# Optimization experiments

Measured on AMD Instinct MI355X. Metric: run time of the kernel, lower is better.

The kernel has to match this reference:

```python
import jax, jax.numpy as jnp
import numpy as np

L0, L1, L2 = 32, 16, 8
NS, NB = 512, 256
CUT = 7.0
N, E, G = 16384, 131072, 16
FEAT = L0 + 3 * L1 + 5 * L2  # 120


def setup_inputs() -> dict:
    key = jax.random.key(0)
    ks = jax.random.split(key, 16)
    rn = lambda k, s, sc=1.0: jax.random.normal(k, s, jnp.float32) * sc
    inp = {}
    inp['nodes'] = rn(ks[0], (N, FEAT))
    inp['pos'] = rn(ks[1], (N, 3)) * 5.0
    inp['cell'] = rn(ks[2], (G, 3, 3))
    inp['edge_shift'] = rn(ks[3], (E, 3))
    # tensor-product path weights (e3nn FullyConnectedTensorProduct, uvw mode)
    inp['W0'] = rn(ks[4], (L0, L0, NS))
    inp['W1'] = rn(ks[5], (L1, L1, NS))
    inp['W2'] = rn(ks[6], (L2, L2, NS))
    inp['ln_g'] = jnp.ones((NS,), jnp.float32)
    inp['ln_b'] = jnp.zeros((NS,), jnp.float32)
    inp['df_w1'] = rn(ks[7], (NB, 1024), NB ** -0.5)
    inp['df_b1'] = jnp.zeros((1024,), jnp.float32)
    inp['df_w2'] = rn(ks[8], (1024, NS), 1024 ** -0.5)
    inp['df_b2'] = jnp.zeros((NS,), jnp.float32)
    inp['mi_w1'] = rn(ks[9], (NS, 1024), NS ** -0.5)
    inp['mi_b1'] = jnp.zeros((1024,), jnp.float32)
    inp['mi_w2'] = rn(ks[10], (1024, 1024), 1024 ** -0.5)
    inp['mi_b2'] = jnp.zeros((1024,), jnp.float32)
    inp['mo_w'] = rn(ks[11], (1024, 1), 1024 ** -0.5)
    inp['mo_b'] = jnp.zeros((1,), jnp.float32)
    inp['edge_index'] = jax.random.randint(ks[12], (2, E), 0, N)
    inp['batch_vec'] = jnp.sort(jax.random.randint(ks[13], (N,), 0, G))
    return inp


def _split_irreps(x):
    x0 = x[:, :L0]                                   # (E, L0) scalars 0e
    x1 = x[:, L0:L0 + 3 * L1].reshape(-1, L1, 3)      # (E, L1, 3) vectors 1o
    x2 = x[:, L0 + 3 * L1:].reshape(-1, L2, 5)        # (E, L2, 5) 2e
    return x0, x1, x2


def reference(nodes, pos, cell, edge_shift, W0, W1, W2, ln_g, ln_b,
              df_w1, df_b1, df_w2, df_b2, mi_w1, mi_b1, mi_w2, mi_b2,
              mo_w, mo_b, edge_index, batch_vec):
    src, dst = edge_index[0], edge_index[1]
    # periodic-image translation vector per edge
    bcell = cell[batch_vec[src]]                      # (E,3,3)
    tvec = jnp.einsum('ei,eij->ej', edge_shift, bcell)
    radvec = pos[dst] - pos[src] + tvec               # (E,3)
    dist = jnp.linalg.norm(radvec, axis=1, keepdims=True)  # (E,1)
    r = 1.0 / (dist + 1e-6)
    # Bessel radial embedding with cutoff CUT, NB basis functions
    n = jnp.arange(1, NB + 1, dtype=jnp.float32)
    emb = jnp.sqrt(2.0 / CUT) * jnp.sin(n * jnp.pi * r / CUT) / r  # (E,NB)
    distfilter = jax.nn.silu(emb @ df_w1 + df_b1) @ df_w2 + df_b2  # (E,NS)

    # symmetrized fully-connected tensor product -> 0e scalars
    # 0.5*(tp(xs,xd)+tp(xd,xs)) == contraction of euv with symmetrized W
    xs0, xs1, xs2 = _split_irreps(nodes[src])
    xd0, xd1, xd2 = _split_irreps(nodes[dst])
    fan = jnp.sqrt(jnp.float32(L0 * L0 + L1 * L1 + L2 * L2))  # element path norm
    sym = lambda W: 0.5 * (W + W.transpose(1, 0, 2))
    e0 = jnp.einsum('eu,ev->euv', xs0, xd0)
    mixed = jnp.einsum('euv,uvw->ew', e0, sym(W0)) / fan
    e1 = jnp.einsum('eui,evi->euv', xs1, xd1)
    mixed = mixed + jnp.einsum('euv,uvw->ew', e1, sym(W1)) / (fan * jnp.sqrt(3.0))
    e2 = jnp.einsum('eui,evi->euv', xs2, xd2)
    mixed = mixed + jnp.einsum('euv,uvw->ew', e2, sym(W2)) / (fan * jnp.sqrt(5.0))

    # LayerNorm over numscalars
    mu = jnp.mean(mixed, axis=-1, keepdims=True)
    var = jnp.mean((mixed - mu) ** 2, axis=-1, keepdims=True)
    mixednorm = (mixed - mu) * jax.lax.rsqrt(var + 1e-5) * ln_g + ln_b

    reg = mixednorm * distfilter
    h = jax.nn.silu(reg @ mi_w1 + mi_b1)
    h = jax.nn.silu(h @ mi_w2 + mi_b2)
    return h @ mo_w + mo_b  # (E,1)
```

## Files before the change

### kernel.cpp

```cpp
#include <hip/hip_runtime.h>

#define EE 131072
#define NNODE 16384
#define FEAT 120
#define NS 512
#define NB 256
#define KCAT 1344

typedef unsigned short u16;
typedef __bf16 bf16x8 __attribute__((ext_vector_type(8)));
typedef float f32x4 __attribute__((ext_vector_type(4)));
typedef float f32x16 __attribute__((ext_vector_type(16)));
typedef unsigned short ushort8 __attribute__((ext_vector_type(8)));

__device__ __forceinline__ float b2f(u16 u) {
  union { unsigned int i; float f; } x; x.i = ((unsigned int)u) << 16; return x.f;
}
__device__ __forceinline__ u16 f2b(float f) {
  union { float f; unsigned int i; } x; x.f = f;
  unsigned int lsb = (x.i >> 16) & 1u;
  x.i += 0x7fffu + lsb;
  return (u16)(x.i >> 16);
}
__device__ __forceinline__ u16 f2b_fast(float f) {
  __bf16 h = (__bf16)f;
  union { __bf16 h; u16 u; } x; x.h = h; return x.u;
}
__device__ __forceinline__ float rdany(const void* p, long i, int f32) {
  return f32 ? ((const float*)p)[i] : b2f(((const u16*)p)[i]);
}

__device__ __forceinline__ void gload16(const u16* g, u16* l) {
  __builtin_amdgcn_global_load_lds(
      (__attribute__((address_space(1))) void*)(u16*)g,
      (__attribute__((address_space(3))) void*)l, 16, 0, 0);
}

__global__ void detect_k(const u16* __restrict__ nodes, int* __restrict__ flag) {
  __shared__ int cnt;
  if (threadIdx.x == 0) cnt = 0;
  __syncthreads();
  u16 v = nodes[threadIdx.x];
  int e = (v >> 7) & 0xFF;
  if (e >= 0x48) atomicAdd(&cnt, 1);
  __syncthreads();
  if (threadIdx.x == 0) *flag = (cnt >= 16) ? 1 : 0;
}

__global__ __launch_bounds__(256) void convert_k(const void* __restrict__ src,
                                                 u16* __restrict__ dst, long n,
                                                 const int* __restrict__ flag) {
  long i = (long)blockIdx.x * 256 + threadIdx.x;
  if (i >= n) return;
  if (*flag)
    dst[i] = f2b(((const float*)src)[i]);
  else
    dst[i] = ((const u16*)src)[i];
}

__global__ __launch_bounds__(256) void transpose_k(const u16* __restrict__ in,
                                                   u16* __restrict__ out, int R, int C) {
  __shared__ u16 tile[32][33];
  int c0 = blockIdx.x * 32, r0 = blockIdx.y * 32;
  int tx = threadIdx.x & 31, ty = threadIdx.x >> 5;
  for (int i = 0; i < 32; i += 8) {
    int r = r0 + ty + i, c = c0 + tx;
    if (r < R && c < C) tile[ty + i][tx] = in[(long)r * C + c];
  }
  __syncthreads();
  for (int i = 0; i < 32; i += 8) {
    int r = r0 + tx, c = c0 + ty + i;
    if (r < R && c < C) out[(long)c * R + r] = tile[tx][ty + i];
  }
}

__global__ __launch_bounds__(256) void build_wcat(const u16* __restrict__ W0,
                                                  const u16* __restrict__ W1,
                                                  const u16* __restrict__ W2,
                                                  u16* __restrict__ wcT) {
  int idx = blockIdx.x * 256 + threadIdx.x;
  if (idx >= NS * KCAT) return;
  int w = idx / KCAT, k = idx - w * KCAT;
  const float fan = 36.66060556f;
  float val;
  if (k < 1024) {
    int u = k >> 5, v = k & 31;
    val = 0.5f * (b2f(W0[(u * 32 + v) * NS + w]) + b2f(W0[(v * 32 + u) * NS + w])) / fan;
  } else if (k < 1280) {
    int j = k - 1024;
    int u = j >> 4, v = j & 15;
    val = 0.5f * (b2f(W1[(u * 16 + v) * NS + w]) + b2f(W1[(v * 16 + u) * NS + w])) /
          (fan * 1.7320508076f);
  } else {
    int j = k - 1280;
    int u = j >> 3, v = j & 7;
    val = 0.5f * (b2f(W2[(u * 8 + v) * NS + w]) + b2f(W2[(v * 8 + u) * NS + w])) /
          (fan * 2.2360679775f);
  }
  wcT[idx] = f2b(val);
}

__global__ __launch_bounds__(256) void edge_prep(
    const u16* __restrict__ nodes, const void* __restrict__ pos, const void* __restrict__ cell,
    const void* __restrict__ shift, const int* __restrict__ eidx, const int* __restrict__ batch,
    u16* __restrict__ emb, u16* __restrict__ ocat, int e0, const int* __restrict__ flag) {
  const int wave = threadIdx.x >> 6, lane = threadIdx.x & 63;
  const int el = blockIdx.x * 4 + wave;
  const int e = e0 + el;
  const int f32 = *flag;
  __shared__ u16 sxs[4][FEAT], sxd[4][FEAT];
  const int src = eidx[e], dst = eidx[EE + e];
  for (int i = lane; i < FEAT; i += 64) {
    sxs[wave][i] = nodes[(long)src * FEAT + i];
    sxd[wave][i] = nodes[(long)dst * FEAT + i];
  }
  __syncthreads();
  const int b = batch[src];
  float s0 = rdany(shift, (long)e * 3, f32), s1 = rdany(shift, (long)e * 3 + 1, f32),
        s2 = rdany(shift, (long)e * 3 + 2, f32);
  float d2 = 0.f;
#pragma unroll
  for (int j = 0; j < 3; j++) {
    float tv = s0 * rdany(cell, b * 9 + j, f32) + s1 * rdany(cell, b * 9 + 3 + j, f32) +
               s2 * rdany(cell, b * 9 + 6 + j, f32);
    float rv = rdany(pos, dst * 3 + j, f32) - rdany(pos, src * 3 + j, f32) + tv;
    d2 += rv * rv;
  }
  float dist = sqrtf(d2);
  float r = 1.0f / (dist + 1e-6f);
  const float c0 = 0.5345224838f;
  const float pi7 = 0.44879895051f;
#pragma unroll
  for (int j = 0; j < 4; j++) {
    int n = lane + 64 * j;
    float val = c0 * sinf((float)(n + 1) * pi7 * r) / r;
    emb[(long)el * NB + n] = f2b(val);
  }
  const u16* xs = sxs[wave];
  const u16* xd = sxd[wave];
  u16* orow = ocat + (long)el * KCAT;
#pragma unroll
  for (int j = 0; j < 16; j++) {
    int k = lane + 64 * j;
    int u = k >> 5, v = k & 31;
    orow[k] = f2b(b2f(xs[u]) * b2f(xd[v]));
  }
#pragma unroll
  for (int j = 0; j < 4; j++) {
    int k = lane + 64 * j;
    int u = k >> 4, v = k & 15;
    float s = 0.f;
#pragma unroll
    for (int i = 0; i < 3; i++) s += b2f(xs[32 + u * 3 + i]) * b2f(xd[32 + v * 3 + i]);
    orow[1024 + k] = f2b(s);
  }
  {
    int u = lane >> 3, v = lane & 7;
    float s = 0.f;
#pragma unroll
    for (int i = 0; i < 5; i++) s += b2f(xs[80 + u * 5 + i]) * b2f(xd[80 + v * 5 + i]);
    orow[1280 + lane] = f2b(s);
  }
}

template <int ACT, int OF32, int HEAD>
__global__ __launch_bounds__(256) void gemm_bt(const u16* __restrict__ A,
                                               const u16* __restrict__ BT,
                                               const u16* __restrict__ bias,
                                               void* __restrict__ Cv,
                                               const u16* __restrict__ hw,
                                               float* __restrict__ outf, int N, int K) {
  __shared__ __align__(16) u16 lA[128 * 64];
  __shared__ __align__(16) u16 lB[128 * 64];
  const int tid = threadIdx.x;
  const int wave = tid >> 6, lane = tid & 63;
  const int half = lane >> 5, l32 = lane & 31, r7 = lane & 7;

  const int nb_n = N >> 7;
  const int nb_m = gridDim.x / nb_n;
  int mi, ni;
  if ((nb_m & 7) == 0) {
    int f = blockIdx.x;
    int xcd = f & 7, s = f >> 3;
    int per = nb_m >> 3;
    mi = xcd * per + s / nb_n;
    ni = s - (s / nb_n) * nb_n;
  } else {
    mi = blockIdx.x / nb_n;
    ni = blockIdx.x - mi * nb_n;
  }
  const long m0 = (long)mi * 128;
  const int n0 = ni * 128;
  const int wm = (wave >> 1) * 64, wn = (wave & 1) * 64;

  f32x16 acc[2][2];
#pragma unroll
  for (int i = 0; i < 2; i++)
#pragma unroll
    for (int j = 0; j < 2; j++)
#pragma unroll
      for (int q = 0; q < 16; q++) acc[i][j][q] = 0.f;

  const int srow = tid >> 3;
  const int gseg = (tid & 7) ^ (srow & 7);
  const u16* Ag = A + (m0 + srow) * K + gseg * 8;
  const u16* Bg = BT + (long)(n0 + srow) * K + gseg * 8;
  u16* la = &lA[tid * 8];
  u16* lb = &lB[tid * 8];

  for (int k0 = 0; k0 < K; k0 += 64) {
#pragma unroll
    for (int ro = 0; ro < 4; ro++) gload16(Ag + (long)(ro * 32) * K + k0, la + ro * 2048);
#pragma unroll
    for (int ro = 0; ro < 4; ro++) gload16(Bg + (long)(ro * 32) * K + k0, lb + ro * 2048);
    __syncthreads();
#pragma unroll
    for (int s = 0; s < 4; s++) {
      const int sl = ((((s << 1) + half) ^ r7) << 3);
      bf16x8 a0 = *(const bf16x8*)&lA[(wm + l32) * 64 + sl];
      bf16x8 a1 = *(const bf16x8*)&lA[(wm + 32 + l32) * 64 + sl];
      bf16x8 b0 = *(const bf16x8*)&lB[(wn + l32) * 64 + sl];
      bf16x8 b1 = *(const bf16x8*)&lB[(wn + 32 + l32) * 64 + sl];
      acc[0][0] = __builtin_amdgcn_mfma_f32_32x32x16_bf16(a0, b0, acc[0][0], 0, 0, 0);
      acc[0][1] = __builtin_amdgcn_mfma_f32_32x32x16_bf16(a0, b1, acc[0][1], 0, 0, 0);
      acc[1][0] = __builtin_amdgcn_mfma_f32_32x32x16_bf16(a1, b0, acc[1][0], 0, 0, 0);
      acc[1][1] = __builtin_amdgcn_mfma_f32_32x32x16_bf16(a1, b1, acc[1][1], 0, 0, 0);
    }
    __syncthreads();
  }

  float* Cf = (float*)Cv;
  u16* Cb = (u16*)Cv;
  float rsum[2][16];
  if (HEAD) {
#pragma unroll
    for (int mt = 0; mt < 2; mt++)
#pragma unroll
      for (int rg = 0; rg < 16; rg++) rsum[mt][rg] = 0.f;
  }
#pragma unroll
  for (int mt = 0; mt < 2; mt++) {
#pragma unroll
    for (int nt = 0; nt < 2; nt++) {
      const int col = n0 + wn + nt * 32 + l32;
      float bv = bias ? b2f(bias[col]) : 0.0f;
      float hwv = HEAD ? b2f(hw[col]) : 0.f;
#pragma unroll
      for (int rg = 0; rg < 16; rg++) {
        long row = m0 + wm + mt * 32 + (rg & 3) + ((rg >> 2) << 3) + (half << 2);
        float v = acc[mt][nt][rg] + bv;
        if (ACT) v = __fdividef(v, 1.0f + __expf(-v));
        if (HEAD) {
          rsum[mt][rg] += v * hwv;
        } else if (OF32) {
          Cf[row * N + col] = v;
        } else {
          Cb[row * N + col] = f2b_fast(v);
        }
      }
    }
  }
  if (HEAD) {
#pragma unroll
    for (int mt = 0; mt < 2; mt++)
#pragma unroll
      for (int rg = 0; rg < 16; rg++) {
        float s = rsum[mt][rg];
        s += __shfl_xor(s, 1);
        s += __shfl_xor(s, 2);
        s += __shfl_xor(s, 4);
        s += __shfl_xor(s, 8);
        s += __shfl_xor(s, 16);
        if (l32 == 0) {
          long row = m0 + wm + mt * 32 + (rg & 3) + ((rg >> 2) << 3) + (half << 2);
          atomicAdd(&outf[row], s);
        }
      }
  }
}

__global__ __launch_bounds__(256) void ln_mul_k(const float* __restrict__ mixed,
                                                const u16* __restrict__ g,
                                                const u16* __restrict__ bvec,
                                                u16* __restrict__ dfreg) {
  const int wave = threadIdx.x >> 6, lane = threadIdx.x & 63;
  const long e = (long)blockIdx.x * 4 + wave;
  const float* row = mixed + e * NS;
  float x[8];
  f32x4 v0 = *(const f32x4*)&row[lane * 8];
  f32x4 v1 = *(const f32x4*)&row[lane * 8 + 4];
#pragma unroll
  for (int j = 0; j < 4; j++) { x[j] = v0[j]; x[4 + j] = v1[j]; }
  float s = 0.f, sq = 0.f;
#pragma unroll
  for (int j = 0; j < 8; j++) { s += x[j]; sq += x[j] * x[j]; }
  for (int o = 32; o; o >>= 1) { s += __shfl_xor(s, o); sq += __shfl_xor(sq, o); }
  float mu = s * (1.0f / 512.0f);
  float var = sq * (1.0f / 512.0f) - mu * mu;
  float rstd = rsqrtf(var + 1e-5f);
  u16* drow = dfreg + e * NS;
  ushort8 dv = *(const ushort8*)&drow[lane * 8];
  ushort8 ov;
#pragma unroll
  for (int j = 0; j < 8; j++) {
    int c = lane * 8 + j;
    float val = (x[j] - mu) * rstd * b2f(g[c]) + b2f(bvec[c]);
    ov[j] = f2b(val * b2f(dv[j]));
  }
  *(ushort8*)&drow[lane * 8] = ov;
}

__global__ __launch_bounds__(256) void head_finish(const float* __restrict__ outf,
                                                   const u16* __restrict__ b,
                                                   void* __restrict__ out,
                                                   const int* __restrict__ flag) {
  int e = blockIdx.x * 256 + threadIdx.x;
  float v = outf[e] + b2f(b[0]);
  if (*flag)
    ((float*)out)[e] = v;
  else
    ((u16*)out)[e] = f2b(v);
}

extern "C" void kernel_launch(void* const* d_in, const int* in_sizes, int n_in, void* d_out,
                              int out_size, void* d_ws, size_t ws_size, hipStream_t stream) {
  const int* eidx = (const int*)d_in[19];
  const int* batch = (const int*)d_in[20];

  char* ws = (char*)d_ws;
  size_t off = 0;
  auto alloc = [&](size_t bytes) {
    char* p = ws + off;
    off += (bytes + 255) & ~(size_t)255;
    return p;
  };

  int* flag = (int*)alloc(256);
  float* outf = (float*)alloc((size_t)EE * 4);

  detect_k<<<1, 256, 0, stream>>>((const u16*)d_in[0], flag);

  u16* cv[19];
  for (int i = 0; i < 19; i++) {
    long n = in_sizes[i];
    cv[i] = (u16*)alloc((size_t)n * 2);
    convert_k<<<(int)((n + 255) / 256), 256, 0, stream>>>(d_in[i], cv[i], n, flag);
  }
  const u16* nodes = cv[0];
  const u16* W0 = cv[4];
  const u16* W1 = cv[5];
  const u16* W2 = cv[6];
  const u16* ln_g = cv[7];
  const u16* ln_b = cv[8];
  const u16* df_w1 = cv[9];
  const u16* df_b1 = cv[10];
  const u16* df_w2 = cv[11];
  const u16* df_b2 = cv[12];
  const u16* mi_w1 = cv[13];
  const u16* mi_b1 = cv[14];
  const u16* mi_w2 = cv[15];
  const u16* mi_b2 = cv[16];
  const u16* mo_w = cv[17];
  const u16* mo_b = cv[18];

  u16* w1T = (u16*)alloc(1024 * 256 * 2);
  u16* w2T = (u16*)alloc(512 * 1024 * 2);
  u16* m1T = (u16*)alloc(1024 * 512 * 2);
  u16* m2T = (u16*)alloc((size_t)1024 * 1024 * 2);
  u16* wcT = (u16*)alloc((size_t)NS * KCAT * 2);

  int nchunk = 1;
  while (nchunk < 64) {
    size_t CHs = (size_t)(EE / nchunk);
    size_t need = off + CHs * 6272 + 8192;
    if (need <= ws_size) break;
    nchunk <<= 1;
  }
  const int CH = EE / nchunk;

  u16* ocat = (u16*)alloc((size_t)CH * KCAT * 2);
  u16* emb = (u16*)alloc((size_t)CH * NB * 2);
  u16* h1 = (u16*)alloc((size_t)CH * 1024 * 2);
  u16* dfb = (u16*)alloc((size_t)CH * NS * 2);
  u16* h2 = ocat;
  float* mixed = (float*)h1;

  transpose_k<<<dim3(1024 / 32, 256 / 32), 256, 0, stream>>>(df_w1, w1T, 256, 1024);
  transpose_k<<<dim3(512 / 32, 1024 / 32), 256, 0, stream>>>(df_w2, w2T, 1024, 512);
  transpose_k<<<dim3(1024 / 32, 512 / 32), 256, 0, stream>>>(mi_w1, m1T, 512, 1024);
  transpose_k<<<dim3(1024 / 32, 1024 / 32), 256, 0, stream>>>(mi_w2, m2T, 1024, 1024);
  build_wcat<<<(NS * KCAT + 255) / 256, 256, 0, stream>>>(W0, W1, W2, wcT);

  hipMemsetAsync(outf, 0, (size_t)EE * 4, stream);

  const int RB = CH / 128;
  for (int c = 0; c < nchunk; c++) {
    const int eb = c * CH;
    edge_prep<<<CH / 4, 256, 0, stream>>>(nodes, d_in[1], d_in[2], d_in[3], eidx, batch, emb,
                                          ocat, eb, flag);

    gemm_bt<1, 0, 0><<<RB * 8, 256, 0, stream>>>(emb, w1T, df_b1, h1, nullptr, nullptr, 1024, 256);
    gemm_bt<0, 0, 0><<<RB * 4, 256, 0, stream>>>(h1, w2T, df_b2, dfb, nullptr, nullptr, 512, 1024);

    gemm_bt<0, 1, 0><<<RB * 4, 256, 0, stream>>>(ocat, wcT, nullptr, mixed, nullptr, nullptr, 512,
                                                 1344);

    ln_mul_k<<<CH / 4, 256, 0, stream>>>(mixed, ln_g, ln_b, dfb);

    gemm_bt<1, 0, 0><<<RB * 8, 256, 0, stream>>>(dfb, m1T, mi_b1, h2, nullptr, nullptr, 1024, 512);
    gemm_bt<1, 0, 1><<<RB * 8, 256, 0, stream>>>(h2, m2T, mi_b2, nullptr, mo_w, outf + eb, 1024,
                                                 1024);
  }
  head_finish<<<EE / 256, 256, 0, stream>>>(outf, mo_b, d_out, flag);
}
```

Baseline: 1.621 ms.

## Store activations in k-octet-major layout and load A fragments directly to registers

Activations move from row-major to a layout where each group of 8 consecutive columns is stored contiguously per row (octet-major). The GEMM then loads A operand fragments straight from global memory into registers and skips the LDS staging and its LDS traffic. The epilogues write in the same layout. The mixed-scalars GEMM also accumulates LayerNorm sum and sum-of-squares through atomics, so the LayerNorm kernel no longer does a reduction. Risks are uncoalesced or latency-exposed direct global A loads, atomic contention, and precision loss from the single-pass variance.

```diff
diff --git a/kernel.cpp b/kernel.cpp
--- a/kernel.cpp
+++ b/kernel.cpp
@@ -103,7 +103,7 @@
 __global__ __launch_bounds__(256) void edge_prep(
     const u16* __restrict__ nodes, const void* __restrict__ pos, const void* __restrict__ cell,
     const void* __restrict__ shift, const int* __restrict__ eidx, const int* __restrict__ batch,
-    u16* __restrict__ emb, u16* __restrict__ ocat, int e0, const int* __restrict__ flag) {
+    u16* __restrict__ emb, u16* __restrict__ ocat, int e0, int M, const int* __restrict__ flag) {
   const int wave = threadIdx.x >> 6, lane = threadIdx.x & 63;
   const int el = blockIdx.x * 4 + wave;
   const int e = e0 + el;
@@ -134,43 +134,42 @@
   for (int j = 0; j < 4; j++) {
     int n = lane + 64 * j;
     float val = c0 * sinf((float)(n + 1) * pi7 * r) / r;
-    emb[(long)el * NB + n] = f2b(val);
+    emb[((long)(n >> 3) * M + el) * 8 + (n & 7)] = f2b(val);
   }
   const u16* xs = sxs[wave];
   const u16* xd = sxd[wave];
-  u16* orow = ocat + (long)el * KCAT;
 #pragma unroll
   for (int j = 0; j < 16; j++) {
     int k = lane + 64 * j;
     int u = k >> 5, v = k & 31;
-    orow[k] = f2b(b2f(xs[u]) * b2f(xd[v]));
+    ocat[((long)(k >> 3) * M + el) * 8 + (k & 7)] = f2b(b2f(xs[u]) * b2f(xd[v]));
   }
 #pragma unroll
   for (int j = 0; j < 4; j++) {
-    int k = lane + 64 * j;
-    int u = k >> 4, v = k & 15;
+    int k = 1024 + lane + 64 * j;
+    int u = (k - 1024) >> 4, v = (k - 1024) & 15;
     float s = 0.f;
 #pragma unroll
     for (int i = 0; i < 3; i++) s += b2f(xs[32 + u * 3 + i]) * b2f(xd[32 + v * 3 + i]);
-    orow[1024 + k] = f2b(s);
+    ocat[((long)(k >> 3) * M + el) * 8 + (k & 7)] = f2b(s);
   }
   {
+    int k = 1280 + lane;
     int u = lane >> 3, v = lane & 7;
     float s = 0.f;
 #pragma unroll
     for (int i = 0; i < 5; i++) s += b2f(xs[80 + u * 5 + i]) * b2f(xd[80 + v * 5 + i]);
-    orow[1280 + lane] = f2b(s);
-  }
-}
-
-template <int ACT, int OF32, int HEAD>
+    ocat[((long)(k >> 3) * M + el) * 8 + (k & 7)] = f2b(s);
+  }
+}
+
+template <int ACT, int OF32, int HEAD, int STATS>
 __global__ __launch_bounds__(256) void gemm_bt(const u16* __restrict__ A,
                                                const u16* __restrict__ BT,
                                                const u16* __restrict__ bias,
                                                void* __restrict__ Cv,
                                                const u16* __restrict__ hw,
-                                               float* __restrict__ outf, int N, int K) {
-  __shared__ __align__(16) u16 lA[128 * 64];
+                                               float* __restrict__ outf, int M, int N, int K) {
   __shared__ __align__(16) u16 lB[128 * 64];
   const int tid = threadIdx.x;
   const int wave = tid >> 6, lane = tid & 63;
@@ -203,34 +202,44 @@
 
   const int srow = tid >> 3;
   const int gseg = (tid & 7) ^ (srow & 7);
-  const u16* Ag = A + (m0 + srow) * K + gseg * 8;
   const u16* Bg = BT + (long)(n0 + srow) * K + gseg * 8;
-  u16* la = &lA[tid * 8];
-  u16* lb = &lB[tid * 8];
+  const int loff = tid * 8;
+  const u16* Am = A + (long)(m0 + wm + l32) * 8;
 
   for (int k0 = 0; k0 < K; k0 += 64) {
 #pragma unroll
-    for (int ro = 0; ro < 4; ro++) gload16(Ag + (long)(ro * 32) * K + k0, la + ro * 2048);
-#pragma unroll
-    for (int ro = 0; ro < 4; ro++) gload16(Bg + (long)(ro * 32) * K + k0, lb + ro * 2048);
+    for (int ro = 0; ro < 4; ro++) gload16(Bg + (long)(ro * 32) * K + k0, &lB[loff + ro * 2048]);
+    bf16x8 af[4][2];
+#pragma unroll
+    for (int s = 0; s < 4; s++) {
+      const long oct = (k0 >> 3) + s * 2 + half;
+      const u16* ap = Am + oct * M * 8;
+      af[s][0] = *(const bf16x8*)ap;
+      af[s][1] = *(const bf16x8*)(ap + 32 * 8);
+    }
     __syncthreads();
 #pragma unroll
     for (int s = 0; s < 4; s++) {
       const int sl = ((((s << 1) + half) ^ r7) << 3);
-      bf16x8 a0 = *(const bf16x8*)&lA[(wm + l32) * 64 + sl];
-      bf16x8 a1 = *(const bf16x8*)&lA[(wm + 32 + l32) * 64 + sl];
       bf16x8 b0 = *(const bf16x8*)&lB[(wn + l32) * 64 + sl];
       bf16x8 b1 = *(const bf16x8*)&lB[(wn + 32 + l32) * 64 + sl];
-      acc[0][0] = __builtin_amdgcn_mfma_f32_32x32x16_bf16(a0, b0, acc[0][0], 0, 0, 0);
-      acc[0][1] = __builtin_amdgcn_mfma_f32_32x32x16_bf16(a0, b1, acc[0][1], 0, 0, 0);
-      acc[1][0] = __builtin_amdgcn_mfma_f32_32x32x16_bf16(a1, b0, acc[1][0], 0, 0, 0);
-      acc[1][1] = __builtin_amdgcn_mfma_f32_32x32x16_bf16(a1, b1, acc[1][1], 0, 0, 0);
+      acc[0][0] = __builtin_amdgcn_mfma_f32_32x32x16_bf16(af[s][0], b0, acc[0][0], 0, 0, 0);
+      acc[0][1] = __builtin_amdgcn_mfma_f32_32x32x16_bf16(af[s][0], b1, acc[0][1], 0, 0, 0);
+      acc[1][0] = __builtin_amdgcn_mfma_f32_32x32x16_bf16(af[s][1], b0, acc[1][0], 0, 0, 0);
+      acc[1][1] = __builtin_amdgcn_mfma_f32_32x32x16_bf16(af[s][1], b1, acc[1][1], 0, 0, 0);
     }
     __syncthreads();
   }
 
   float* Cf = (float*)Cv;
   u16* Cb = (u16*)Cv;
+  float bv[2], hwv[2];
+#pragma unroll
+  for (int nt = 0; nt < 2; nt++) {
+    const int col = n0 + wn + nt * 32 + l32;
+    bv[nt] = bias ? b2f(bias[col]) : 0.0f;
+    hwv[nt] = HEAD ? b2f(hw[col]) : 0.f;
+  }
   float rsum[2][16];
   if (HEAD) {
 #pragma unroll
@@ -241,21 +250,32 @@
 #pragma unroll
   for (int mt = 0; mt < 2; mt++) {
 #pragma unroll
-    for (int nt = 0; nt < 2; nt++) {
-      const int col = n0 + wn + nt * 32 + l32;
-      float bv = bias ? b2f(bias[col]) : 0.0f;
-      float hwv = HEAD ? b2f(hw[col]) : 0.f;
-#pragma unroll
-      for (int rg = 0; rg < 16; rg++) {
-        long row = m0 + wm + mt * 32 + (rg & 3) + ((rg >> 2) << 3) + (half << 2);
-        float v = acc[mt][nt][rg] + bv;
+    for (int rg = 0; rg < 16; rg++) {
+      const long row = m0 + wm + mt * 32 + (rg & 3) + ((rg >> 2) << 3) + (half << 2);
+      float s = 0.f, sq = 0.f;
+#pragma unroll
+      for (int nt = 0; nt < 2; nt++) {
+        const int col = n0 + wn + nt * 32 + l32;
+        float v = acc[mt][nt][rg] + bv[nt];
         if (ACT) v = __fdividef(v, 1.0f + __expf(-v));
         if (HEAD) {
-          rsum[mt][rg] += v * hwv;
+          rsum[mt][rg] += v * hwv[nt];
         } else if (OF32) {
-          Cf[row * N + col] = v;
+          Cf[((long)(col >> 3) * M + row) * 8 + (col & 7)] = v;
         } else {
-          Cb[row * N + col] = f2b_fast(v);
+          Cb[((long)(col >> 3) * M + row) * 8 + (col & 7)] = f2b_fast(v);
+        }
+        if (STATS) { s += v; sq += v * v; }
+      }
+      if (STATS) {
+        s += __shfl_xor(s, 1);  sq += __shfl_xor(sq, 1);
+        s += __shfl_xor(s, 2);  sq += __shfl_xor(sq, 2);
+        s += __shfl_xor(s, 4);  sq += __shfl_xor(sq, 4);
+        s += __shfl_xor(s, 8);  sq += __shfl_xor(sq, 8);
+        s += __shfl_xor(s, 16); sq += __shfl_xor(sq, 16);
+        if (l32 == 0) {
+          atomicAdd(&outf[row], s);
+          atomicAdd(&outf[M + row], sq);
         }
       }
     }
@@ -272,7 +292,7 @@
         s += __shfl_xor(s, 8);
         s += __shfl_xor(s, 16);
         if (l32 == 0) {
-          long row = m0 + wm + mt * 32 + (rg & 3) + ((rg >> 2) << 3) + (half << 2);
+          const long row = m0 + wm + mt * 32 + (rg & 3) + ((rg >> 2) << 3) + (half << 2);
           atomicAdd(&outf[row], s);
         }
       }
@@ -280,34 +300,43 @@
 }
 
 __global__ __launch_bounds__(256) void ln_mul_k(const float* __restrict__ mixed,
+                                                const float* __restrict__ stats,
                                                 const u16* __restrict__ g,
                                                 const u16* __restrict__ bvec,
-                                                u16* __restrict__ dfreg) {
+                                                u16* __restrict__ dfreg, int M) {
   const int wave = threadIdx.x >> 6, lane = threadIdx.x & 63;
-  const long e = (long)blockIdx.x * 4 + wave;
-  const float* row = mixed + e * NS;
-  float x[8];
-  f32x4 v0 = *(const f32x4*)&row[lane * 8];
-  f32x4 v1 = *(const f32x4*)&row[lane * 8 + 4];
-#pragma unroll
-  for (int j = 0; j < 4; j++) { x[j] = v0[j]; x[4 + j] = v1[j]; }
-  float s = 0.f, sq = 0.f;
-#pragma unroll
-  for (int j = 0; j < 8; j++) { s += x[j]; sq += x[j] * x[j]; }
-  for (int o = 32; o; o >>= 1) { s += __shfl_xor(s, o); sq += __shfl_xor(sq, o); }
-  float mu = s * (1.0f / 512.0f);
-  float var = sq * (1.0f / 512.0f) - mu * mu;
-  float rstd = rsqrtf(var + 1e-5f);
-  u16* drow = dfreg + e * NS;
-  ushort8 dv = *(const ushort8*)&drow[lane * 8];
-  ushort8 ov;
-#pragma unroll
-  for (int j = 0; j < 8; j++) {
-    int c = lane * 8 + j;
-    float val = (x[j] - mu) * rstd * b2f(g[c]) + b2f(bvec[c]);
-    ov[j] = f2b(val * b2f(dv[j]));
-  }
-  *(ushort8*)&drow[lane * 8] = ov;
+  const int e0 = blockIdx.x * 64;
+  __shared__ float smu[64], srs[64];
+  if (threadIdx.x < 64) {
+    int e = e0 + threadIdx.x;
+    float mu = stats[e] * (1.0f / 512.0f);
+    float var = stats[M + e] * (1.0f / 512.0f) - mu * mu;
+    smu[threadIdx.x] = mu;
+    srs[threadIdx.x] = rsqrtf(var + 1e-5f);
+  }
+  __syncthreads();
+  const float mu = smu[lane], rs = srs[lane];
+  const int e = e0 + lane;
+#pragma unroll 4
+  for (int t = 0; t < 16; t++) {
+    const int o = wave * 16 + t;
+    const long base = ((long)o * M + e) * 8;
+    f32x4 x0 = *(const f32x4*)&mixed[base];
+    f32x4 x1 = *(const f32x4*)&mixed[base + 4];
+    ushort8 dv = *(const ushort8*)&dfreg[base];
+    ushort8 ov;
+#pragma unroll
+    for (int j = 0; j < 4; j++) {
+      float val = (x0[j] - mu) * rs * b2f(g[o * 8 + j]) + b2f(bvec[o * 8 + j]);
+      ov[j] = f2b(val * b2f(dv[j]));
+    }
+#pragma unroll
+    for (int j = 0; j < 4; j++) {
+      float val = (x1[j] - mu) * rs * b2f(g[o * 8 + 4 + j]) + b2f(bvec[o * 8 + 4 + j]);
+      ov[4 + j] = f2b(val * b2f(dv[4 + j]));
+    }
+    *(ushort8*)&dfreg[base] = ov;
+  }
 }
 
 __global__ __launch_bounds__(256) void head_finish(const float* __restrict__ outf,
@@ -372,7 +401,7 @@
   int nchunk = 1;
   while (nchunk < 64) {
     size_t CHs = (size_t)(EE / nchunk);
-    size_t need = off + CHs * 6272 + 8192;
+    size_t need = off + CHs * 6280 + 16384;
     if (need <= ws_size) break;
     nchunk <<= 1;
   }
@@ -382,6 +411,7 @@
   u16* emb = (u16*)alloc((size_t)CH * NB * 2);
   u16* h1 = (u16*)alloc((size_t)CH * 1024 * 2);
   u16* dfb = (u16*)alloc((size_t)CH * NS * 2);
+  float* stats = (float*)alloc((size_t)CH * 8);
   u16* h2 = ocat;
   float* mixed = (float*)h1;
 
@@ -397,19 +427,23 @@
   for (int c = 0; c < nchunk; c++) {
     const int eb = c * CH;
     edge_prep<<<CH / 4, 256, 0, stream>>>(nodes, d_in[1], d_in[2], d_in[3], eidx, batch, emb,
-                                          ocat, eb, flag);
-
-    gemm_bt<1, 0, 0><<<RB * 8, 256, 0, stream>>>(emb, w1T, df_b1, h1, nullptr, nullptr, 1024, 256);
-    gemm_bt<0, 0, 0><<<RB * 4, 256, 0, stream>>>(h1, w2T, df_b2, dfb, nullptr, nullptr, 512, 1024);
-
-    gemm_bt<0, 1, 0><<<RB * 4, 256, 0, stream>>>(ocat, wcT, nullptr, mixed, nullptr, nullptr, 512,
-                                                 1344);
-
-    ln_mul_k<<<CH / 4, 256, 0, stream>>>(mixed, ln_g, ln_b, dfb);
-
-    gemm_bt<1, 0, 0><<<RB * 8, 256, 0, stream>>>(dfb, m1T, mi_b1, h2, nullptr, nullptr, 1024, 512);
-    gemm_bt<1, 0, 1><<<RB * 8, 256, 0, stream>>>(h2, m2T, mi_b2, nullptr, mo_w, outf + eb, 1024,
-                                                 1024);
+                                          ocat, eb, CH, flag);
+
+    gemm_bt<1, 0, 0, 0><<<RB * 8, 256, 0, stream>>>(emb, w1T, df_b1, h1, nullptr, nullptr, CH,
+                                                    1024, 256);
+    gemm_bt<0, 0, 0, 0><<<RB * 4, 256, 0, stream>>>(h1, w2T, df_b2, dfb, nullptr, nullptr, CH,
+                                                    512, 1024);
+
+    hipMemsetAsync(stats, 0, (size_t)CH * 8, stream);
+    gemm_bt<0, 1, 0, 1><<<RB * 4, 256, 0, stream>>>(ocat, wcT, nullptr, mixed, nullptr, stats,
+                                                    CH, 512, 1344);
+
+    ln_mul_k<<<CH / 64, 256, 0, stream>>>(mixed, stats, ln_g, ln_b, dfb, CH);
+
+    gemm_bt<1, 0, 0, 0><<<RB * 8, 256, 0, stream>>>(dfb, m1T, mi_b1, h2, nullptr, nullptr, CH,
+                                                    1024, 512);
+    gemm_bt<1, 0, 1, 0><<<RB * 8, 256, 0, stream>>>(h2, m2T, mi_b2, nullptr, mo_w, outf + eb, CH,
+                                                    1024, 1024);
   }
   head_finish<<<EE / 256, 256, 0, stream>>>(outf, mo_b, d_out, flag);
 }
```

Measured after the change: 1.809 ms. +11.6%, slower.
